# Kernel optimization log

Measured on AMD Instinct MI355X. Metric: run time of the kernel, lower is better.

## Reference

```python
import jax, jax.numpy as jnp
import numpy as np

N, E, D = 50000, 800000, 128   # nodes, edges, hidden dim (in_dim == out_dim == 128)
MSG_EPS = 1e-7                 # GENConv eps added to relu(msg)
SM_EPS = 1e-16                 # PyG softmax denominator eps


def _glorotish(key, shape, fan_in):
    return jax.random.normal(key, shape, jnp.float32) * (1.0 / np.sqrt(fan_in))


def setup_inputs() -> dict:
    key = jax.random.key(0)
    ks = jax.random.split(key, 8)
    return dict(
        x=jax.random.normal(ks[0], (N, D), jnp.float32),
        edge_index=jax.random.randint(ks[1], (2, E), 0, N),
        edge_attr=jax.random.uniform(ks[2], (E, 1), jnp.float32),
        # GENConv params (bias=False internals, per PyG defaults)
        W_edge=_glorotish(ks[3], (D, 1), 1),          # lin_edge: edge_dim=1 -> D
        t=jnp.array(1.0, jnp.float32),                # learnable softmax temperature
        W1=_glorotish(ks[4], (2 * D, D), D),          # MLP: D -> 2D
        bn_gamma=jnp.ones((2 * D,), jnp.float32),     # BatchNorm1d affine
        bn_beta=jnp.zeros((2 * D,), jnp.float32),
        W2=_glorotish(ks[5], (D, 2 * D), 2 * D),      # MLP: 2D -> D
        # outer LayerNorm
        ln_gamma=jnp.ones((D,), jnp.float32),
        ln_beta=jnp.zeros((D,), jnp.float32),
        # edge_mlp: Linear(2D -> D) + GELU + LayerNorm
        We=_glorotish(ks[6], (D, 2 * D), 2 * D),
        be=jnp.zeros((D,), jnp.float32),
        ln_e_gamma=jnp.ones((D,), jnp.float32),
        ln_e_beta=jnp.zeros((D,), jnp.float32),
    )


def layer_norm(x, g, b, eps=1e-5):
    mu = x.mean(-1, keepdims=True)
    var = x.var(-1, keepdims=True)
    return (x - mu) * jax.lax.rsqrt(var + eps) * g + b


def reference(x, edge_index, edge_attr, W_edge, t, W1, bn_gamma, bn_beta, W2,
              ln_gamma, ln_beta, We, be, ln_e_gamma, ln_e_beta):
    src, dst = edge_index[0], edge_index[1]

    # --- GENConv ---
    e = edge_attr @ W_edge.T                                  # [E, D] lin_edge
    msg = jax.nn.relu(x[src] + e) + MSG_EPS                   # [E, D] message

    # per-destination scatter-softmax (per channel), temperature t
    scores = msg * t
    smax = jax.ops.segment_max(scores, dst, num_segments=N)   # [N, D]
    ex = jnp.exp(scores - smax[dst])
    denom = jax.ops.segment_sum(ex, dst, num_segments=N)      # [N, D]
    alpha = ex / (denom[dst] + SM_EPS)
    aggr = jax.ops.segment_sum(msg * alpha, dst, num_segments=N)  # [N, D]

    h = aggr + x                                              # residual (in==out dim)

    # GENConv MLP: Linear -> BatchNorm(batch stats) -> ReLU -> Linear
    h1 = h @ W1.T                                             # [N, 2D]
    mu = h1.mean(0)
    var = h1.var(0)
    h1 = (h1 - mu) * jax.lax.rsqrt(var + 1e-5) * bn_gamma + bn_beta
    h1 = jax.nn.relu(h1)
    out_conv = h1 @ W2.T                                      # [N, D]

    # --- wrapper: LayerNorm + ELU (dropout = eval identity) ---
    out_x = jax.nn.elu(layer_norm(out_conv, ln_gamma, ln_beta))

    # --- edge_mlp: gather-concat -> Linear -> GELU -> LayerNorm ---
    edge_feat = jnp.concatenate([out_x[src], out_x[dst]], axis=1)  # [E, 2D]
    out_e = layer_norm(jax.nn.gelu(edge_feat @ We.T + be, approximate=False),
                       ln_e_gamma, ln_e_beta)                 # [E, D]
    return out_x, out_e
```

## Files before the change

kernel.cpp:

```cpp
#include <hip/hip_runtime.h>
#include <math.h>

typedef _Float16 f16;
typedef _Float16 f16x4 __attribute__((ext_vector_type(4)));
typedef _Float16 f16x8 __attribute__((ext_vector_type(8)));
typedef float f32x4 __attribute__((ext_vector_type(4)));

#define DIVUP(a, b) (((a) + (b) - 1) / (b))


__global__ __launch_bounds__(256) void k_hist(const int* __restrict__ dst, int* __restrict__ deg, int E) {
    int i = blockIdx.x * 256 + threadIdx.x;
    if (i < E) atomicAdd(&deg[dst[i]], 1);
}

__global__ __launch_bounds__(256) void k_scan_block(const int* __restrict__ deg, int* __restrict__ tmp,
                                                    int* __restrict__ bsum, int n) {
    __shared__ int sh[256];
    int i = blockIdx.x * 256 + threadIdx.x;
    int v = (i < n) ? deg[i] : 0;
    sh[threadIdx.x] = v;
    __syncthreads();
    #pragma unroll
    for (int off = 1; off < 256; off <<= 1) {
        int t = (threadIdx.x >= off) ? sh[threadIdx.x - off] : 0;
        __syncthreads();
        sh[threadIdx.x] += t;
        __syncthreads();
    }
    if (i < n) tmp[i] = sh[threadIdx.x];
    if (threadIdx.x == 255) bsum[blockIdx.x] = sh[255];
}

__global__ __launch_bounds__(256) void k_scan_bsum(const int* __restrict__ bsum, int* __restrict__ bsum_ex, int nb) {
    __shared__ int sh[256];
    int t = threadIdx.x;
    int v = (t < nb) ? bsum[t] : 0;
    sh[t] = v;
    __syncthreads();
    #pragma unroll
    for (int off = 1; off < 256; off <<= 1) {
        int u = (t >= off) ? sh[t - off] : 0;
        __syncthreads();
        sh[t] += u;
        __syncthreads();
    }
    bsum_ex[t] = sh[t] - v;
}

__global__ __launch_bounds__(256) void k_scan_finish(const int* __restrict__ tmp, const int* __restrict__ deg,
                                                     const int* __restrict__ bsum_ex, int* __restrict__ offs,
                                                     int* __restrict__ cursor, int n) {
    int i = blockIdx.x * 256 + threadIdx.x;
    if (i < n) {
        int ex = tmp[i] - deg[i] + bsum_ex[blockIdx.x];
        offs[i] = ex;
        cursor[i] = ex;
    }
}

__global__ __launch_bounds__(256) void k_scatter(const int* __restrict__ src, const int* __restrict__ dst,
                                                 const float* __restrict__ ea, int* __restrict__ cursor,
                                                 int2* __restrict__ perm, int E) {
    int i = blockIdx.x * 256 + threadIdx.x;
    if (i < E) {
        int d = dst[i];
        int pos = atomicAdd(&cursor[d], 1);
        perm[pos] = make_int2(src[i], __float_as_int(ea[i]));
    }
}

__global__ __launch_bounds__(128) void k_aggr_h(const int* __restrict__ offs, const int* __restrict__ deg,
                                                const int2* __restrict__ perm,
                                                const float* __restrict__ x, const float* __restrict__ W_edge,
                                                const float* __restrict__ t_ptr, float* __restrict__ h, int n) {
    int node = blockIdx.x;
    int d = threadIdx.x;
    float t = *t_ptr;
    float we = W_edge[d];
    int start = offs[node], cnt = deg[node];
    float denom = 0.f, numer = 0.f;
    for (int e = 0; e < cnt; ++e) {
        int2 pe = perm[start + e];
        int s = pe.x;
        float ea = __int_as_float(pe.y);
        float m = fmaxf(x[(size_t)s * 128 + d] + ea * we, 0.f) + 1e-7f;
        float es = __expf(m * t);
        denom += es;
        numer += m * es;
    }
    h[(size_t)node * 128 + d] = numer / (denom + 1e-16f) + x[(size_t)node * 128 + d];
}

__global__ __launch_bounds__(256) void k_prep(const float* __restrict__ W1, const float* __restrict__ W2,
                                              const float* __restrict__ We, f16* __restrict__ B1,
                                              f16* __restrict__ B2, f16* __restrict__ BM) {
    int i = blockIdx.x * 256 + threadIdx.x;
    if (i < 32768) {
        B1[i] = (f16)W1[i];
    } else if (i < 65536) {
        int j = i - 32768;
        B2[j] = (f16)W2[j];
    } else {
        int j = i - 65536;
        int jj = j >> 7, d = j & 127;
        BM[j] = (f16)((jj < 128) ? We[jj * 256 + d] : We[(jj - 128) * 256 + 128 + d]);
    }
}

template <int KTOT, int MODE>
__global__ __launch_bounds__(256) void k_gemm(const float* __restrict__ A, const f16* __restrict__ Bg,
                                              float* __restrict__ Cout, int nrows,
                                              float* __restrict__ colsum, float* __restrict__ colsq,
                                              const float* __restrict__ bnscale, const float* __restrict__ bnshift,
                                              const float* __restrict__ lng, const float* __restrict__ lnb) {
    __shared__ f16 As[128 * 136];
    __shared__ f16 Bs[128 * 136];
    __shared__ float Ssum[2][128];
    __shared__ float Sq[2][128];
    const int tid = threadIdx.x;
    const int lane = tid & 63, w = tid >> 6;
    const int m = lane & 15, quad = lane >> 4;
    const int row0 = blockIdx.x * 128, col0 = blockIdx.y * 128;
    const int wrow = (w & 1) * 64, wcol = (w >> 1) * 64;
    f32x4 acc[4][4] = {};

    for (int kc = 0; kc < KTOT; kc += 128) {
        if (kc) __syncthreads();
        #pragma unroll
        for (int q = 0; q < 16; q++) {
            int f = tid + q * 256;
            int r = f >> 5, c4 = f & 31;
            int gr = row0 + r;
            float4 v = (gr < nrows) ? *(const float4*)(A + (size_t)gr * KTOT + kc + c4 * 4)
                                    : make_float4(0.f, 0.f, 0.f, 0.f);
            if (MODE == 1) {
                float4 sc = *(const float4*)(bnscale + kc + c4 * 4);
                float4 sh = *(const float4*)(bnshift + kc + c4 * 4);
                v.x = fmaxf(fmaf(v.x, sc.x, sh.x), 0.f);
                v.y = fmaxf(fmaf(v.y, sc.y, sh.y), 0.f);
                v.z = fmaxf(fmaf(v.z, sc.z, sh.z), 0.f);
                v.w = fmaxf(fmaf(v.w, sc.w, sh.w), 0.f);
            }
            f16x4 hv = {(f16)v.x, (f16)v.y, (f16)v.z, (f16)v.w};
            *(f16x4*)(As + r * 136 + c4 * 4) = hv;
        }
        #pragma unroll
        for (int q = 0; q < 8; q++) {
            int f = tid + q * 256;
            int r = f >> 4, k8 = f & 15;
            *(uint4*)(Bs + r * 136 + k8 * 8) =
                *(const uint4*)(Bg + (size_t)(col0 + r) * KTOT + kc + k8 * 8);
        }
        __syncthreads();
        #pragma unroll
        for (int k0 = 0; k0 < 128; k0 += 32) {
            f16x8 a[4], b[4];
            #pragma unroll
            for (int i = 0; i < 4; i++)
                a[i] = *(const f16x8*)(As + (wrow + i * 16 + m) * 136 + k0 + quad * 8);
            #pragma unroll
            for (int j = 0; j < 4; j++)
                b[j] = *(const f16x8*)(Bs + (wcol + j * 16 + m) * 136 + k0 + quad * 8);
            #pragma unroll
            for (int i = 0; i < 4; i++)
                #pragma unroll
                for (int j = 0; j < 4; j++)
                    acc[i][j] = __builtin_amdgcn_mfma_f32_16x16x32_f16(a[i], b[j], acc[i][j], 0, 0, 0);
        }
    }

    if (MODE == 0 || MODE == 2) {
        #pragma unroll
        for (int i = 0; i < 4; i++)
            #pragma unroll
            for (int r = 0; r < 4; r++) {
                int grow = row0 + wrow + i * 16 + quad * 4 + r;
                if (grow < nrows) {
                    #pragma unroll
                    for (int j = 0; j < 4; j++)
                        Cout[(size_t)grow * 256 + col0 + wcol + j * 16 + m] = acc[i][j][r];
                }
            }
    }
    if (MODE == 0) {
        #pragma unroll
        for (int j = 0; j < 4; j++) {
            float s = 0.f, qq = 0.f;
            #pragma unroll
            for (int i = 0; i < 4; i++)
                #pragma unroll
                for (int r = 0; r < 4; r++) {
                    float v = acc[i][j][r];
                    s += v;
                    qq += v * v;
                }
            s += __shfl_xor(s, 16); s += __shfl_xor(s, 32);
            qq += __shfl_xor(qq, 16); qq += __shfl_xor(qq, 32);
            if (lane < 16) {
                atomicAdd(&colsum[col0 + wcol + j * 16 + lane], s);
                atomicAdd(&colsq[col0 + wcol + j * 16 + lane], qq);
            }
        }
    }
    if (MODE == 1) {
        const int cw = w >> 1;
        #pragma unroll
        for (int i = 0; i < 4; i++)
            #pragma unroll
            for (int r = 0; r < 4; r++) {
                float s = 0.f, qq = 0.f;
                #pragma unroll
                for (int j = 0; j < 4; j++) {
                    float v = acc[i][j][r];
                    s += v;
                    qq += v * v;
                }
                s += __shfl_xor(s, 1); s += __shfl_xor(s, 2);
                s += __shfl_xor(s, 4); s += __shfl_xor(s, 8);
                qq += __shfl_xor(qq, 1); qq += __shfl_xor(qq, 2);
                qq += __shfl_xor(qq, 4); qq += __shfl_xor(qq, 8);
                if (m == 0) {
                    int lrow = wrow + i * 16 + quad * 4 + r;
                    Ssum[cw][lrow] = s;
                    Sq[cw][lrow] = qq;
                }
            }
        __syncthreads();
        float lg[4], lb[4];
        #pragma unroll
        for (int j = 0; j < 4; j++) {
            lg[j] = lng[wcol + j * 16 + m];
            lb[j] = lnb[wcol + j * 16 + m];
        }
        #pragma unroll
        for (int i = 0; i < 4; i++)
            #pragma unroll
            for (int r = 0; r < 4; r++) {
                int lrow = wrow + i * 16 + quad * 4 + r;
                int grow = row0 + lrow;
                if (grow < nrows) {
                    float S = Ssum[0][lrow] + Ssum[1][lrow];
                    float Q = Sq[0][lrow] + Sq[1][lrow];
                    float mu = S * (1.f / 128.f);
                    float var = Q * (1.f / 128.f) - mu * mu;
                    float rs = rsqrtf(var + 1e-5f);
                    #pragma unroll
                    for (int j = 0; j < 4; j++) {
                        float v = (acc[i][j][r] - mu) * rs * lg[j] + lb[j];
                        v = v > 0.f ? v : expm1f(v);
                        Cout[(size_t)grow * 128 + wcol + j * 16 + m] = v;
                    }
                }
            }
    }
}

__global__ __launch_bounds__(256) void k_bn_finish(const float* __restrict__ colsum, const float* __restrict__ colsq,
                                                   const float* __restrict__ g, const float* __restrict__ b,
                                                   float* __restrict__ scale, float* __restrict__ shift, float invN) {
    int j = threadIdx.x;
    float mu = colsum[j] * invN;
    float var = colsq[j] * invN - mu * mu;
    float sc = g[j] * rsqrtf(var + 1e-5f);
    scale[j] = sc;
    shift[j] = b[j] - mu * sc;
}

__global__ __launch_bounds__(256) void k_edge_out(const int* __restrict__ src, const int* __restrict__ dst,
                                                  const float* __restrict__ CAB, const float* __restrict__ be,
                                                  const float* __restrict__ lng, const float* __restrict__ lnb,
                                                  float* __restrict__ oute, int E) {
    int e = blockIdx.x * 4 + (threadIdx.x >> 6);
    int lane = threadIdx.x & 63;
    if (e >= E) return;
    int s = src[e], d = dst[e];
    int k = lane * 2;
    float2 va = *(const float2*)(CAB + (size_t)s * 256 + k);
    float2 vb = *(const float2*)(CAB + (size_t)d * 256 + 128 + k);
    float2 bb = *(const float2*)(be + k);
    float x0 = va.x + vb.x + bb.x;
    float x1 = va.y + vb.y + bb.y;
    const float is2 = 0.70710678118654752f;
    float g0 = 0.5f * x0 * (1.f + erff(x0 * is2));
    float g1 = 0.5f * x1 * (1.f + erff(x1 * is2));
    float s1 = g0 + g1, s2 = g0 * g0 + g1 * g1;
    #pragma unroll
    for (int off = 32; off; off >>= 1) {
        s1 += __shfl_xor(s1, off);
        s2 += __shfl_xor(s2, off);
    }
    float mu = s1 * (1.f / 128.f);
    float var = s2 * (1.f / 128.f) - mu * mu;
    float rs = rsqrtf(var + 1e-5f);
    float2 gg = *(const float2*)(lng + k);
    float2 b2 = *(const float2*)(lnb + k);
    float o0 = (g0 - mu) * rs * gg.x + b2.x;
    float o1 = (g1 - mu) * rs * gg.y + b2.y;
    *(float2*)(oute + (size_t)e * 128 + k) = make_float2(o0, o1);
}

extern "C" void kernel_launch(void* const* d_in, const int* in_sizes, int n_in,
                              void* d_out, int out_size, void* d_ws, size_t ws_size,
                              hipStream_t stream) {
    const int N = in_sizes[0] / 128;
    const int E = in_sizes[1] / 2;

    const float* x      = (const float*)d_in[0];
    const int*   ei     = (const int*)d_in[1];
    const int*   src    = ei;
    const int*   dst    = ei + E;
    const float* ea     = (const float*)d_in[2];
    const float* W_edge = (const float*)d_in[3];
    const float* t_ptr  = (const float*)d_in[4];
    const float* W1     = (const float*)d_in[5];
    const float* bng    = (const float*)d_in[6];
    const float* bnb    = (const float*)d_in[7];
    const float* W2     = (const float*)d_in[8];
    const float* lng    = (const float*)d_in[9];
    const float* lnb    = (const float*)d_in[10];
    const float* We     = (const float*)d_in[11];
    const float* be     = (const float*)d_in[12];
    const float* lneg   = (const float*)d_in[13];
    const float* lneb   = (const float*)d_in[14];

    float* out_x = (float*)d_out;
    float* out_e = out_x + (size_t)N * 128;

    float* h = (float*)d_ws;
    float* C = h + (size_t)N * 128;
    int2*  perm     = (int2*)C;
    int*   deg      = (int*)(perm + E);
    int*   offs     = deg + N;
    int*   cursor   = offs + N;
    int*   tmp      = cursor + N;
    int*   bsum     = tmp + N;
    int*   bsum_ex  = bsum + 256;
    float* small    = C + (size_t)N * 256;
    float* colsum   = small;
    float* colsq    = small + 256;
    float* bnscale  = small + 512;
    float* bnshift  = small + 768;
    f16*   B1f16    = (f16*)(small + 1024);
    f16*   B2f16    = B1f16 + 32768;
    f16*   BMf16    = B2f16 + 32768;

    const int EB = DIVUP(E, 256);
    const int NB = DIVUP(N, 256);
    const int GR = DIVUP(N, 128);

    hipMemsetAsync(deg, 0, (size_t)N * sizeof(int), stream);
    hipMemsetAsync(colsum, 0, 512 * sizeof(float), stream);

    k_prep<<<384, 256, 0, stream>>>(W1, W2, We, B1f16, B2f16, BMf16);

    k_hist<<<EB, 256, 0, stream>>>(dst, deg, E);
    k_scan_block<<<NB, 256, 0, stream>>>(deg, tmp, bsum, N);
    k_scan_bsum<<<1, 256, 0, stream>>>(bsum, bsum_ex, NB);
    k_scan_finish<<<NB, 256, 0, stream>>>(tmp, deg, bsum_ex, offs, cursor, N);
    k_scatter<<<EB, 256, 0, stream>>>(src, dst, ea, cursor, perm, E);

    k_aggr_h<<<N, 128, 0, stream>>>(offs, deg, perm, x, W_edge, t_ptr, h, N);

    k_gemm<128, 0><<<dim3(GR, 2), 256, 0, stream>>>(h, B1f16, C, N, colsum, colsq,
                                                    nullptr, nullptr, nullptr, nullptr);
    k_bn_finish<<<1, 256, 0, stream>>>(colsum, colsq, bng, bnb, bnscale, bnshift, 1.0f / (float)N);
    k_gemm<256, 1><<<dim3(GR, 1), 256, 0, stream>>>(C, B2f16, out_x, N, nullptr, nullptr,
                                                    bnscale, bnshift, lng, lnb);

    k_gemm<128, 2><<<dim3(GR, 2), 256, 0, stream>>>(out_x, BMf16, C, N, nullptr, nullptr,
                                                    nullptr, nullptr, nullptr, nullptr);
    k_edge_out<<<DIVUP(E, 4), 256, 0, stream>>>(src, dst, C, be, lneg, lneb, out_e, E);
}
```

Baseline: 915.0 us.

## Store intermediates in fp16 and iterate edge output per destination node

```diff
diff --git a/kernel.cpp b/kernel.cpp
--- a/kernel.cpp
+++ b/kernel.cpp
@@ -2,6 +2,7 @@
 #include <math.h>
 
 typedef _Float16 f16;
+typedef _Float16 f16x2 __attribute__((ext_vector_type(2)));
 typedef _Float16 f16x4 __attribute__((ext_vector_type(4)));
 typedef _Float16 f16x8 __attribute__((ext_vector_type(8)));
 typedef float f32x4 __attribute__((ext_vector_type(4)));
@@ -61,19 +62,29 @@
 
 __global__ __launch_bounds__(256) void k_scatter(const int* __restrict__ src, const int* __restrict__ dst,
                                                  const float* __restrict__ ea, int* __restrict__ cursor,
-                                                 int2* __restrict__ perm, int E) {
+                                                 int4* __restrict__ perm, int E) {
     int i = blockIdx.x * 256 + threadIdx.x;
     if (i < E) {
         int d = dst[i];
         int pos = atomicAdd(&cursor[d], 1);
-        perm[pos] = make_int2(src[i], __float_as_int(ea[i]));
+        perm[pos] = make_int4(src[i], __float_as_int(ea[i]), i, 0);
+    }
+}
+
+__global__ __launch_bounds__(256) void k_xhalf(const float* __restrict__ x, f16* __restrict__ xh, int n4) {
+    int i = blockIdx.x * 256 + threadIdx.x;
+    if (i < n4) {
+        float4 v = ((const float4*)x)[i];
+        f16x4 hv = {(f16)v.x, (f16)v.y, (f16)v.z, (f16)v.w};
+        ((f16x4*)xh)[i] = hv;
     }
 }
 
 __global__ __launch_bounds__(128) void k_aggr_h(const int* __restrict__ offs, const int* __restrict__ deg,
-                                                const int2* __restrict__ perm,
-                                                const float* __restrict__ x, const float* __restrict__ W_edge,
-                                                const float* __restrict__ t_ptr, float* __restrict__ h, int n) {
+                                                const int4* __restrict__ perm,
+                                                const float* __restrict__ x, const f16* __restrict__ xh,
+                                                const float* __restrict__ W_edge,
+                                                const float* __restrict__ t_ptr, f16* __restrict__ h, int n) {
     int node = blockIdx.x;
     int d = threadIdx.x;
     float t = *t_ptr;
@@ -81,15 +92,15 @@
     int start = offs[node], cnt = deg[node];
     float denom = 0.f, numer = 0.f;
     for (int e = 0; e < cnt; ++e) {
-        int2 pe = perm[start + e];
-        int s = pe.x;
+        int4 pe = perm[start + e];
+        float xv = (float)xh[(size_t)pe.x * 128 + d];
         float ea = __int_as_float(pe.y);
-        float m = fmaxf(x[(size_t)s * 128 + d] + ea * we, 0.f) + 1e-7f;
+        float m = fmaxf(xv + ea * we, 0.f) + 1e-7f;
         float es = __expf(m * t);
         denom += es;
         numer += m * es;
     }
-    h[(size_t)node * 128 + d] = numer / (denom + 1e-16f) + x[(size_t)node * 128 + d];
+    h[(size_t)node * 128 + d] = (f16)(numer / (denom + 1e-16f) + x[(size_t)node * 128 + d]);
 }
 
 __global__ __launch_bounds__(256) void k_prep(const float* __restrict__ W1, const float* __restrict__ W2,
@@ -109,7 +120,7 @@
 }
 
 template <int KTOT, int MODE>
-__global__ __launch_bounds__(256) void k_gemm(const float* __restrict__ A, const f16* __restrict__ Bg,
+__global__ __launch_bounds__(256) void k_gemm(const void* __restrict__ Av, const f16* __restrict__ Bg,
                                               float* __restrict__ Cout, int nrows,
                                               float* __restrict__ colsum, float* __restrict__ colsq,
                                               const float* __restrict__ bnscale, const float* __restrict__ bnshift,
@@ -127,23 +138,36 @@
 
     for (int kc = 0; kc < KTOT; kc += 128) {
         if (kc) __syncthreads();
-        #pragma unroll
-        for (int q = 0; q < 16; q++) {
-            int f = tid + q * 256;
-            int r = f >> 5, c4 = f & 31;
-            int gr = row0 + r;
-            float4 v = (gr < nrows) ? *(const float4*)(A + (size_t)gr * KTOT + kc + c4 * 4)
-                                    : make_float4(0.f, 0.f, 0.f, 0.f);
-            if (MODE == 1) {
-                float4 sc = *(const float4*)(bnscale + kc + c4 * 4);
-                float4 sh = *(const float4*)(bnshift + kc + c4 * 4);
-                v.x = fmaxf(fmaf(v.x, sc.x, sh.x), 0.f);
-                v.y = fmaxf(fmaf(v.y, sc.y, sh.y), 0.f);
-                v.z = fmaxf(fmaf(v.z, sc.z, sh.z), 0.f);
-                v.w = fmaxf(fmaf(v.w, sc.w, sh.w), 0.f);
-            }
-            f16x4 hv = {(f16)v.x, (f16)v.y, (f16)v.z, (f16)v.w};
-            *(f16x4*)(As + r * 136 + c4 * 4) = hv;
+        if (MODE == 2) {
+            const float* A = (const float*)Av;
+            #pragma unroll
+            for (int q = 0; q < 16; q++) {
+                int f = tid + q * 256;
+                int r = f >> 5, c4 = f & 31;
+                int gr = row0 + r;
+                float4 v = (gr < nrows) ? *(const float4*)(A + (size_t)gr * KTOT + kc + c4 * 4)
+                                        : make_float4(0.f, 0.f, 0.f, 0.f);
+                f16x4 hv = {(f16)v.x, (f16)v.y, (f16)v.z, (f16)v.w};
+                *(f16x4*)(As + r * 136 + c4 * 4) = hv;
+            }
+        } else {
+            const f16* Ah = (const f16*)Av;
+            #pragma unroll
+            for (int q = 0; q < 8; q++) {
+                int f = tid + q * 256;
+                int r = f >> 4, k8 = f & 15;
+                int gr = row0 + r;
+                f16x8 hv = {};
+                if (gr < nrows) hv = *(const f16x8*)(Ah + (size_t)gr * KTOT + kc + k8 * 8);
+                if (MODE == 1) {
+                    const float* sc = bnscale + kc + k8 * 8;
+                    const float* sh = bnshift + kc + k8 * 8;
+                    #pragma unroll
+                    for (int u = 0; u < 8; u++)
+                        hv[u] = (f16)fmaxf(fmaf((float)hv[u], sc[u], sh[u]), 0.f);
+                }
+                *(f16x8*)(As + r * 136 + k8 * 8) = hv;
+            }
         }
         #pragma unroll
         for (int q = 0; q < 8; q++) {
@@ -171,6 +195,7 @@
     }
 
     if (MODE == 0 || MODE == 2) {
+        f16* Ch = (f16*)Cout;
         #pragma unroll
         for (int i = 0; i < 4; i++)
             #pragma unroll
@@ -179,7 +204,7 @@
                 if (grow < nrows) {
                     #pragma unroll
                     for (int j = 0; j < 4; j++)
-                        Cout[(size_t)grow * 256 + col0 + wcol + j * 16 + m] = acc[i][j][r];
+                        Ch[(size_t)grow * 256 + col0 + wcol + j * 16 + m] = (f16)acc[i][j][r];
                 }
             }
     }
@@ -267,37 +292,48 @@
     shift[j] = b[j] - mu * sc;
 }
 
-__global__ __launch_bounds__(256) void k_edge_out(const int* __restrict__ src, const int* __restrict__ dst,
-                                                  const float* __restrict__ CAB, const float* __restrict__ be,
+__global__ __launch_bounds__(256) void k_edge_out(const int* __restrict__ offs, const int* __restrict__ deg,
+                                                  const int4* __restrict__ perm, const f16* __restrict__ CAB,
+                                                  const float* __restrict__ be,
                                                   const float* __restrict__ lng, const float* __restrict__ lnb,
-                                                  float* __restrict__ oute, int E) {
-    int e = blockIdx.x * 4 + (threadIdx.x >> 6);
+                                                  float* __restrict__ oute, int N) {
+    int node = blockIdx.x * 4 + (threadIdx.x >> 6);
     int lane = threadIdx.x & 63;
-    if (e >= E) return;
-    int s = src[e], d = dst[e];
+    if (node >= N) return;
+    int cnt = deg[node];
+    if (cnt == 0) return;
+    int start = offs[node];
     int k = lane * 2;
-    float2 va = *(const float2*)(CAB + (size_t)s * 256 + k);
-    float2 vb = *(const float2*)(CAB + (size_t)d * 256 + 128 + k);
+    f16x2 vb = *(const f16x2*)(CAB + (size_t)node * 256 + 128 + k);
     float2 bb = *(const float2*)(be + k);
-    float x0 = va.x + vb.x + bb.x;
-    float x1 = va.y + vb.y + bb.y;
-    const float is2 = 0.70710678118654752f;
-    float g0 = 0.5f * x0 * (1.f + erff(x0 * is2));
-    float g1 = 0.5f * x1 * (1.f + erff(x1 * is2));
-    float s1 = g0 + g1, s2 = g0 * g0 + g1 * g1;
-    #pragma unroll
-    for (int off = 32; off; off >>= 1) {
-        s1 += __shfl_xor(s1, off);
-        s2 += __shfl_xor(s2, off);
-    }
-    float mu = s1 * (1.f / 128.f);
-    float var = s2 * (1.f / 128.f) - mu * mu;
-    float rs = rsqrtf(var + 1e-5f);
+    float bx = (float)vb.x + bb.x;
+    float by = (float)vb.y + bb.y;
     float2 gg = *(const float2*)(lng + k);
     float2 b2 = *(const float2*)(lnb + k);
-    float o0 = (g0 - mu) * rs * gg.x + b2.x;
-    float o1 = (g1 - mu) * rs * gg.y + b2.y;
-    *(float2*)(oute + (size_t)e * 128 + k) = make_float2(o0, o1);
+    const float is2 = 0.70710678118654752f;
+
+    int4 pe = perm[start];
+    for (int e = 0; e < cnt; ++e) {
+        int4 pen = (e + 1 < cnt) ? perm[start + e + 1] : pe;
+        f16x2 va = *(const f16x2*)(CAB + (size_t)pe.x * 256 + k);
+        float x0 = (float)va.x + bx;
+        float x1 = (float)va.y + by;
+        float g0 = 0.5f * x0 * (1.f + erff(x0 * is2));
+        float g1 = 0.5f * x1 * (1.f + erff(x1 * is2));
+        float s1 = g0 + g1, s2 = g0 * g0 + g1 * g1;
+        #pragma unroll
+        for (int off = 32; off; off >>= 1) {
+            s1 += __shfl_xor(s1, off);
+            s2 += __shfl_xor(s2, off);
+        }
+        float mu = s1 * (1.f / 128.f);
+        float var = s2 * (1.f / 128.f) - mu * mu;
+        float rs = rsqrtf(var + 1e-5f);
+        float o0 = (g0 - mu) * rs * gg.x + b2.x;
+        float o1 = (g1 - mu) * rs * gg.y + b2.y;
+        *(float2*)(oute + (size_t)pe.z * 128 + k) = make_float2(o0, o1);
+        pe = pen;
+    }
 }
 
 extern "C" void kernel_launch(void* const* d_in, const int* in_sizes, int n_in,
@@ -327,23 +363,24 @@
     float* out_x = (float*)d_out;
     float* out_e = out_x + (size_t)N * 128;
 
-    float* h = (float*)d_ws;
-    float* C = h + (size_t)N * 128;
-    int2*  perm     = (int2*)C;
-    int*   deg      = (int*)(perm + E);
-    int*   offs     = deg + N;
-    int*   cursor   = offs + N;
-    int*   tmp      = cursor + N;
-    int*   bsum     = tmp + N;
-    int*   bsum_ex  = bsum + 256;
-    float* small    = C + (size_t)N * 256;
-    float* colsum   = small;
-    float* colsq    = small + 256;
-    float* bnscale  = small + 512;
-    float* bnshift  = small + 768;
-    f16*   B1f16    = (f16*)(small + 1024);
-    f16*   B2f16    = B1f16 + 32768;
-    f16*   BMf16    = B2f16 + 32768;
+    f16*   h   = (f16*)d_ws;
+    f16*   xh  = h + (size_t)N * 128;
+    f16*   C   = xh + (size_t)N * 128;
+    int4*  perm    = (int4*)(C + (size_t)N * 256);
+    int*   deg     = (int*)(perm + E);
+    int*   offs    = deg + N;
+    int*   cursor  = offs + N;
+    int*   tmp     = cursor + N;
+    int*   bsum    = tmp + N;
+    int*   bsum_ex = bsum + 256;
+    float* small   = (float*)(bsum_ex + 256);
+    float* colsum  = small;
+    float* colsq   = small + 256;
+    float* bnscale = small + 512;
+    float* bnshift = small + 768;
+    f16*   B1f16   = (f16*)(small + 1024);
+    f16*   B2f16   = B1f16 + 32768;
+    f16*   BMf16   = B2f16 + 32768;
 
     const int EB = DIVUP(E, 256);
     const int NB = DIVUP(N, 256);
@@ -353,6 +390,7 @@
     hipMemsetAsync(colsum, 0, 512 * sizeof(float), stream);
 
     k_prep<<<384, 256, 0, stream>>>(W1, W2, We, B1f16, B2f16, BMf16);
+    k_xhalf<<<DIVUP(N * 32, 256), 256, 0, stream>>>(x, xh, N * 32);
 
     k_hist<<<EB, 256, 0, stream>>>(dst, deg, E);
     k_scan_block<<<NB, 256, 0, stream>>>(deg, tmp, bsum, N);
@@ -360,15 +398,15 @@
     k_scan_finish<<<NB, 256, 0, stream>>>(tmp, deg, bsum_ex, offs, cursor, N);
     k_scatter<<<EB, 256, 0, stream>>>(src, dst, ea, cursor, perm, E);
 
-    k_aggr_h<<<N, 128, 0, stream>>>(offs, deg, perm, x, W_edge, t_ptr, h, N);
-
-    k_gemm<128, 0><<<dim3(GR, 2), 256, 0, stream>>>(h, B1f16, C, N, colsum, colsq,
+    k_aggr_h<<<N, 128, 0, stream>>>(offs, deg, perm, x, xh, W_edge, t_ptr, h, N);
+
+    k_gemm<128, 0><<<dim3(GR, 2), 256, 0, stream>>>(h, B1f16, (float*)C, N, colsum, colsq,
                                                     nullptr, nullptr, nullptr, nullptr);
     k_bn_finish<<<1, 256, 0, stream>>>(colsum, colsq, bng, bnb, bnscale, bnshift, 1.0f / (float)N);
     k_gemm<256, 1><<<dim3(GR, 1), 256, 0, stream>>>(C, B2f16, out_x, N, nullptr, nullptr,
                                                     bnscale, bnshift, lng, lnb);
 
-    k_gemm<128, 2><<<dim3(GR, 2), 256, 0, stream>>>(out_x, BMf16, C, N, nullptr, nullptr,
+    k_gemm<128, 2><<<dim3(GR, 2), 256, 0, stream>>>(out_x, BMf16, (float*)C, N, nullptr, nullptr,
                                                     nullptr, nullptr, nullptr, nullptr);
-    k_edge_out<<<DIVUP(E, 4), 256, 0, stream>>>(src, dst, C, be, lneg, lneb, out_e, E);
-}
+    k_edge_out<<<DIVUP(N, 4), 256, 0, stream>>>(offs, deg, perm, C, be, lneg, lneb, out_e, E > 0 ? N : 0);
+}
```

New measurement: 891.4 us. 2.6% less time.
